# Kernel tuning notes

Measured on AMD Instinct MI355X. Metric: run time of the kernel, lower is better.

The kernel has to match this reference:

```python
import jax, jax.numpy as jnp
import numpy as np

EPS = 1e-6

def _conv(x, w, padding):
    # x: [B,C,H,W], w: [O,I,kh,kw]
    return jax.lax.conv_general_dilated(x, w, window_strides=(1, 1), padding=padding,
                                        dimension_numbers=('NCHW', 'OIHW', 'NCHW'))

def setup_inputs() -> dict:
    key = jax.random.key(0)
    ks = jax.random.split(key, 8)
    C = 512
    B, H, W = 4, 64, 64
    s1 = 1.0 / np.sqrt(C)          # 1x1 conv fan-in
    s3 = 1.0 / np.sqrt(C * 9)      # 3x3 conv fan-in
    return {
        'x': jax.random.normal(ks[0], (B, C, H, W), dtype=jnp.float32),
        'ln_w': jnp.ones((C,), dtype=jnp.float32),
        'ln_b': jnp.zeros((C,), dtype=jnp.float32),
        'wq': jax.random.normal(ks[1], (C, C, 1, 1), dtype=jnp.float32) * s1,
        'wk': jax.random.normal(ks[2], (C, C, 3, 3), dtype=jnp.float32) * s3,
        'wv': jax.random.normal(ks[3], (C, C, 3, 3), dtype=jnp.float32) * s3,
        'wp': jax.random.normal(ks[4], (C, C, 1, 1), dtype=jnp.float32) * s1,
        'bp': jnp.zeros((C,), dtype=jnp.float32),
    }

def reference(x, ln_w, ln_b, wq, wk, wv, wp, bp):
    # channels_first LayerNorm over C
    u = jnp.mean(x, axis=1, keepdims=True)
    s = jnp.mean((x - u) ** 2, axis=1, keepdims=True)
    h = (x - u) / jnp.sqrt(s + EPS)
    h = ln_w[None, :, None, None] * h + ln_b[None, :, None, None]

    q = _conv(h, wq, 'VALID')           # 1x1
    k = _conv(h, wk, [(1, 1), (1, 1)])  # 3x3, pad 1
    v = _conv(h, wv, [(1, 1), (1, 1)])

    b, c, H, W = q.shape
    hw = H * W
    q = q.reshape(b, c, hw)
    k = k.reshape(b, c, hw)
    v = v.reshape(b, c, hw)

    scale = jnp.asarray(int(c) ** (-0.5), q.dtype)
    attn = jnp.einsum('bcm,bcn->bmn', q, k) * scale  # [b, hw_q, hw_k]
    attn = jax.nn.softmax(attn, axis=2)
    out = jnp.einsum('bcn,bmn->bcm', v, attn)        # [b, c, hw_q]
    out = out.reshape(b, c, H, W)

    out = _conv(out, wp, 'VALID') + bp[None, :, None, None]
    return x + out
```

## Files before the change

### kernel.cpp

```cpp
#include <hip/hip_runtime.h>
#include <hip/hip_bf16.h>

#define C_DIM 512
#define HW    4096
#define BATCH 4
#define PW    66
#define PPIX  (PW*PW)

typedef __attribute__((ext_vector_type(8))) short bf16x8;
typedef __attribute__((ext_vector_type(4))) float f32x4;
typedef __attribute__((ext_vector_type(16))) float f32x16;
typedef __attribute__((ext_vector_type(2))) long long l64x2;

static __device__ __forceinline__ short f2b(float f) {
    union { float f; unsigned u; } v; v.f = f;
    unsigned r = v.u + 0x7fffu + ((v.u >> 16) & 1u);
    return (short)(r >> 16);
}
static __device__ __forceinline__ float b2f(short s) {
    union { unsigned u; float f; } v; v.u = ((unsigned)(unsigned short)s) << 16;
    return v.f;
}

static __device__ __forceinline__ f32x4 zero4() {
    f32x4 v = {0.f, 0.f, 0.f, 0.f};
    return v;
}
static __device__ __forceinline__ f32x16 zero16() {
    f32x16 v = {0.f,0.f,0.f,0.f, 0.f,0.f,0.f,0.f, 0.f,0.f,0.f,0.f, 0.f,0.f,0.f,0.f};
    return v;
}

static __device__ __forceinline__ void gload16(const void* g, void* l) {
    __builtin_amdgcn_global_load_lds(
        (__attribute__((address_space(1))) void*)g,
        (__attribute__((address_space(3))) void*)l, 16, 0, 0);
}

__global__ void k_reorder_w38(const float* __restrict__ w, unsigned char* __restrict__ out) {
    int i = blockIdx.x * 256 + threadIdx.x;
    int o = i / 576;
    int p8 = (i - o * 576) * 8;
    int kc2 = p8 >> 6;
    int tap = kc2 >> 3;
    int p = p8 & 63;
    int g = (p >> 4) & 3, half = (p >> 3) & 1;
    int c0 = (kc2 & 7) * 64 + half * 32 + g * 8;
    const float* src = w + ((size_t)o * 512 + c0) * 9 + tap;
    float f0 = src[0] * 64.f, f1 = src[9] * 64.f, f2 = src[18] * 64.f, f3 = src[27] * 64.f;
    float f4 = src[36] * 64.f, f5 = src[45] * 64.f, f6 = src[54] * 64.f, f7 = src[63] * 64.f;
    int lo = __builtin_amdgcn_cvt_pk_fp8_f32(f0, f1, 0, false);
    lo     = __builtin_amdgcn_cvt_pk_fp8_f32(f2, f3, lo, true);
    int hi = __builtin_amdgcn_cvt_pk_fp8_f32(f4, f5, 0, false);
    hi     = __builtin_amdgcn_cvt_pk_fp8_f32(f6, f7, hi, true);
    *(uint2*)&out[(size_t)o * 4608 + p8] = make_uint2((unsigned)lo, (unsigned)hi);
}

__global__ void k_reorder_w18(const float* __restrict__ w, unsigned char* __restrict__ out) {
    int i = blockIdx.x * 256 + threadIdx.x;
    int o = i >> 6;
    int p8 = (i & 63) * 8;
    int grp = p8 >> 6;
    int p = p8 & 63;
    int g = (p >> 4) & 3, half = (p >> 3) & 1;
    int c0 = grp * 64 + half * 32 + g * 8;
    const float* src = w + (size_t)o * 512 + c0;
    int lo = __builtin_amdgcn_cvt_pk_fp8_f32(src[0] * 64.f, src[1] * 64.f, 0, false);
    lo     = __builtin_amdgcn_cvt_pk_fp8_f32(src[2] * 64.f, src[3] * 64.f, lo, true);
    int hi = __builtin_amdgcn_cvt_pk_fp8_f32(src[4] * 64.f, src[5] * 64.f, 0, false);
    hi     = __builtin_amdgcn_cvt_pk_fp8_f32(src[6] * 64.f, src[7] * 64.f, hi, true);
    *(uint2*)&out[(size_t)o * 512 + p8] = make_uint2((unsigned)lo, (unsigned)hi);
}

__global__ void k_cvt_k8(const short* __restrict__ in, unsigned char* __restrict__ out) {
    int i = blockIdx.x * 256 + threadIdx.x;
    int m = i >> 6;
    int p = (i & 63) * 8;
    int kcp = p >> 6, g = (p >> 4) & 3, half = (p >> 3) & 1;
    int chb = (kcp * 2 + half) * 32 + g * 8;
    bf16x8 v = *(const bf16x8*)&in[(size_t)m * 512 + chb];
    int lo = __builtin_amdgcn_cvt_pk_fp8_f32(b2f(v[0]), b2f(v[1]), 0, false);
    lo     = __builtin_amdgcn_cvt_pk_fp8_f32(b2f(v[2]), b2f(v[3]), lo, true);
    int hi = __builtin_amdgcn_cvt_pk_fp8_f32(b2f(v[4]), b2f(v[5]), 0, false);
    hi     = __builtin_amdgcn_cvt_pk_fp8_f32(b2f(v[6]), b2f(v[7]), hi, true);
    *(uint2*)&out[(size_t)m * 512 + p] = make_uint2((unsigned)lo, (unsigned)hi);
}

__global__ void k_ln_fused(const float* __restrict__ x, const float* __restrict__ lnw,
                           const float* __restrict__ lnb, unsigned char* __restrict__ hp8) {
    __shared__ float red[8][64];
    __shared__ float mean_s[64], rstd_s[64];
    __shared__ short tile[64][65];
    int bid = blockIdx.x;
    int y = bid & 63, b = bid >> 6;
    int t = threadIdx.x;
    int px = t & 63, cg = t >> 6;
    const float* xb = x + (size_t)b * C_DIM * HW + (size_t)y * 64;

    float s = 0.f, sq = 0.f;
    for (int c = cg * 128; c < cg * 128 + 128; ++c) {
        float v = xb[(size_t)c * HW + px];
        s += v; sq += v * v;
    }
    red[cg][px] = s;
    red[4 + cg][px] = sq;
    __syncthreads();
    if (t < 64) {
        float S = red[0][t] + red[1][t] + red[2][t] + red[3][t];
        float Q = red[4][t] + red[5][t] + red[6][t] + red[7][t];
        float mu  = S * (1.0f / C_DIM);
        float var = Q * (1.0f / C_DIM) - mu * mu;
        mean_s[t] = mu;
        rstd_s[t] = 1.0f / sqrtf(var + 1e-6f);
    }
    __syncthreads();
    float mu = mean_s[px], rs = rstd_s[px];
    int chn = t & 7, pxe = t >> 3;
    int clocal = (chn & 1) * 32 + ((chn >> 1) & 3) * 8;
    for (int ct = 0; ct < 8; ++ct) {
        int c0 = ct * 64;
        #pragma unroll
        for (int cc = 0; cc < 64; cc += 4) {
            int c = c0 + cc + cg;
            float v = xb[(size_t)c * HW + px];
            tile[cc + cg][px] = f2b((v - mu) * rs * lnw[c] + lnb[c]);
        }
        __syncthreads();
        #pragma unroll
        for (int h = 0; h < 2; ++h) {
            int pix = pxe + h * 32;
            float f0 = b2f(tile[clocal + 0][pix]);
            float f1 = b2f(tile[clocal + 1][pix]);
            float f2 = b2f(tile[clocal + 2][pix]);
            float f3 = b2f(tile[clocal + 3][pix]);
            float f4 = b2f(tile[clocal + 4][pix]);
            float f5 = b2f(tile[clocal + 5][pix]);
            float f6 = b2f(tile[clocal + 6][pix]);
            float f7 = b2f(tile[clocal + 7][pix]);
            int lo = __builtin_amdgcn_cvt_pk_fp8_f32(f0, f1, 0, false);
            lo     = __builtin_amdgcn_cvt_pk_fp8_f32(f2, f3, lo, true);
            int hi = __builtin_amdgcn_cvt_pk_fp8_f32(f4, f5, 0, false);
            hi     = __builtin_amdgcn_cvt_pk_fp8_f32(f6, f7, hi, true);
            size_t row = (size_t)b * PPIX + (size_t)(y + 1) * PW + 1 + pix;
            *(uint2*)&hp8[row * 512 + c0 + chn * 8] = make_uint2((unsigned)lo, (unsigned)hi);
        }
        __syncthreads();
    }
}

__global__ __launch_bounds__(256, 2) void k_gemm_kv8(
        const unsigned char* __restrict__ A8, const unsigned char* __restrict__ Bk8,
        const unsigned char* __restrict__ Bv8, short* __restrict__ OutK,
        short* __restrict__ OutV)
{
    __shared__ unsigned char Alds[2][10240];
    __shared__ unsigned char Bklds[2][10240];
    __shared__ unsigned char Bvlds[2][10240];
    int bid = blockIdx.x;
    int mt = bid & 31, nt = (bid >> 5) & 3, b = bid >> 7;
    int m0 = mt * 128, n0 = nt * 128;
    int t = threadIdx.x;
    int lane = t & 63, w = t >> 6;
    int wm = w >> 1, wn = w & 1;
    int g = lane >> 4, li = lane & 15;
    const unsigned char* Ab = A8 + (size_t)b * PPIX * 512;

    int srowv[3], schv[3];
    #pragma unroll
    for (int r = 0; r < 3; ++r) {
        int slot = r * 256 + t;
        int row = slot / 5;
        int ch = slot - row * 5;
        srowv[r] = row;
        schv[r] = (ch < 4) ? ch * 16 : 0;
    }
    bool act2 = (w < 2);

    f32x4 accK[4][4], accV[4][4];
    #pragma unroll
    for (int i = 0; i < 4; ++i)
        #pragma unroll
        for (int j = 0; j < 4; ++j) { accK[i][j] = zero4(); accV[i][j] = zero4(); }

    auto STAGE = [&](int bf, int kc2) {
        int tap = kc2 >> 3;
        int gofs = (kc2 & 7) * 64;
        int ty3 = tap / 3, tx3 = tap % 3;
        #pragma unroll
        for (int r = 0; r < 3; ++r) {
            if (r < 2 || act2) {
                int row = srowv[r];
                int m = m0 + row;
                int yy = m >> 6, xx = m & 63;
                int pp = (yy + ty3) * PW + xx + tx3;
                int dst = (r * 256 + t) * 16;
                gload16(Ab + (size_t)pp * 512 + gofs + schv[r], &Alds[bf][dst]);
                size_t gb = (size_t)(n0 + row) * 4608 + kc2 * 64 + schv[r];
                gload16(Bk8 + gb, &Bklds[bf][dst]);
                gload16(Bv8 + gb, &Bvlds[bf][dst]);
            }
        }
    };

    auto COMPUTE = [&](int bf) {
        l64x2 av[4], bk[4], bv[4];
        #pragma unroll
        for (int i = 0; i < 4; ++i)
            av[i] = *(const l64x2*)&Alds[bf][(wm * 64 + i * 16 + li) * 80 + g * 16];
        #pragma unroll
        for (int j = 0; j < 4; ++j)
            bk[j] = *(const l64x2*)&Bklds[bf][(wn * 64 + j * 16 + li) * 80 + g * 16];
        #pragma unroll
        for (int j = 0; j < 4; ++j)
            bv[j] = *(const l64x2*)&Bvlds[bf][(wn * 64 + j * 16 + li) * 80 + g * 16];
        #pragma unroll
        for (int h = 0; h < 2; ++h) {
            #pragma unroll
            for (int i = 0; i < 4; ++i)
                #pragma unroll
                for (int j = 0; j < 4; ++j)
                    accK[i][j] = __builtin_amdgcn_mfma_f32_16x16x32_fp8_fp8(
                        av[i][h], bk[j][h], accK[i][j], 0, 0, 0);
            #pragma unroll
            for (int i = 0; i < 4; ++i)
                #pragma unroll
                for (int j = 0; j < 4; ++j)
                    accV[i][j] = __builtin_amdgcn_mfma_f32_16x16x32_fp8_fp8(
                        av[i][h], bv[j][h], accV[i][j], 0, 0, 0);
        }
    };

    STAGE(0, 0);
    __syncthreads();
    int bf = 0;
    for (int kc2 = 0; kc2 < 72; ++kc2) {
        if (kc2 + 1 < 72) STAGE(bf ^ 1, kc2 + 1);
        COMPUTE(bf);
        __syncthreads();
        bf ^= 1;
    }

    const float SCL = 0.015625f;
    #pragma unroll
    for (int fm = 0; fm < 4; ++fm) {
        #pragma unroll
        for (int fn = 0; fn < 4; ++fn) {
            int mrow = m0 + wm * 64 + fm * 16 + g * 4;
            int ncol = n0 + wn * 64 + fn * 16 + li;
            #pragma unroll
            for (int i = 0; i < 4; ++i) {
                size_t dst = ((size_t)b * HW + mrow + i) * C_DIM + ncol;
                OutK[dst] = f2b(accK[fm][fn][i] * SCL);
            }
            size_t dstv = ((size_t)b * C_DIM + ncol) * HW + mrow;
            short4 sv = make_short4(f2b(accV[fm][fn][0] * SCL), f2b(accV[fm][fn][1] * SCL),
                                    f2b(accV[fm][fn][2] * SCL), f2b(accV[fm][fn][3] * SCL));
            *(short4*)(OutV + dstv) = sv;
        }
    }
}

__global__ __launch_bounds__(256, 2) void k_gemm_q8(
        const unsigned char* __restrict__ A8, const unsigned char* __restrict__ Bq8,
        short* __restrict__ OutQ)
{
    __shared__ unsigned char Alds[2][10240];
    __shared__ unsigned char Blds[2][10240];
    int bid = blockIdx.x;
    int mt = bid & 31, nt = (bid >> 5) & 3, b = bid >> 7;
    int m0 = mt * 128, n0 = nt * 128;
    int t = threadIdx.x;
    int lane = t & 63, w = t >> 6;
    int wm = w >> 1, wn = w & 1;
    int g = lane >> 4, li = lane & 15;
    const unsigned char* Ab = A8 + (size_t)b * PPIX * 512;

    int srowv[3], schv[3];
    #pragma unroll
    for (int r = 0; r < 3; ++r) {
        int slot = r * 256 + t;
        int row = slot / 5;
        int ch = slot - row * 5;
        srowv[r] = row;
        schv[r] = (ch < 4) ? ch * 16 : 0;
    }
    bool act2 = (w < 2);

    f32x4 accQ[4][4];
    #pragma unroll
    for (int i = 0; i < 4; ++i)
        #pragma unroll
        for (int j = 0; j < 4; ++j) accQ[i][j] = zero4();

    auto STAGE = [&](int bf, int kc2) {
        int gofs = kc2 * 64;
        #pragma unroll
        for (int r = 0; r < 3; ++r) {
            if (r < 2 || act2) {
                int row = srowv[r];
                int m = m0 + row;
                int yy = m >> 6, xx = m & 63;
                int pp = (yy + 1) * PW + xx + 1;
                int dst = (r * 256 + t) * 16;
                gload16(Ab + (size_t)pp * 512 + gofs + schv[r], &Alds[bf][dst]);
                gload16(Bq8 + (size_t)(n0 + row) * 512 + gofs + schv[r], &Blds[bf][dst]);
            }
        }
    };

    auto COMPUTE = [&](int bf) {
        l64x2 av[4], bq[4];
        #pragma unroll
        for (int i = 0; i < 4; ++i)
            av[i] = *(const l64x2*)&Alds[bf][(wm * 64 + i * 16 + li) * 80 + g * 16];
        #pragma unroll
        for (int j = 0; j < 4; ++j)
            bq[j] = *(const l64x2*)&Blds[bf][(wn * 64 + j * 16 + li) * 80 + g * 16];
        #pragma unroll
        for (int h = 0; h < 2; ++h)
            #pragma unroll
            for (int i = 0; i < 4; ++i)
                #pragma unroll
                for (int j = 0; j < 4; ++j)
                    accQ[i][j] = __builtin_amdgcn_mfma_f32_16x16x32_fp8_fp8(
                        av[i][h], bq[j][h], accQ[i][j], 0, 0, 0);
    };

    STAGE(0, 0);
    __syncthreads();
    int bf = 0;
    for (int kc2 = 0; kc2 < 8; ++kc2) {
        if (kc2 + 1 < 8) STAGE(bf ^ 1, kc2 + 1);
        COMPUTE(bf);
        __syncthreads();
        bf ^= 1;
    }

    const float SCL = 0.015625f;
    #pragma unroll
    for (int fm = 0; fm < 4; ++fm) {
        #pragma unroll
        for (int fn = 0; fn < 4; ++fn) {
            int mrow = m0 + wm * 64 + fm * 16 + g * 4;
            int ncol = n0 + wn * 64 + fn * 16 + li;
            #pragma unroll
            for (int i = 0; i < 4; ++i) {
                size_t dst = ((size_t)b * HW + mrow + i) * C_DIM + ncol;
                OutQ[dst] = f2b(accQ[fm][fn][i] * SCL);
            }
        }
    }
}

__global__ __launch_bounds__(256, 2) void k_gemm_p8(
        const unsigned char* __restrict__ A8, const unsigned char* __restrict__ Bp8,
        float* __restrict__ Out, const float* __restrict__ bias,
        const float* __restrict__ resid)
{
    __shared__ unsigned char Alds[2][10240];
    __shared__ unsigned char Blds[2][10240];
    int bid = blockIdx.x;
    int mt = bid & 31, nt = (bid >> 5) & 3, b = bid >> 7;
    int m0 = mt * 128, n0 = nt * 128;
    int t = threadIdx.x;
    int lane = t & 63, w = t >> 6;
    int wm = w >> 1, wn = w & 1;
    int g = lane >> 4, li = lane & 15;
    const unsigned char* Ab = A8 + (size_t)b * HW * 512;

    int srowv[3], schv[3];
    #pragma unroll
    for (int r = 0; r < 3; ++r) {
        int slot = r * 256 + t;
        int row = slot / 5;
        int ch = slot - row * 5;
        srowv[r] = row;
        schv[r] = (ch < 4) ? ch * 16 : 0;
    }
    bool act2 = (w < 2);

    f32x4 acc[4][4];
    #pragma unroll
    for (int i = 0; i < 4; ++i)
        #pragma unroll
        for (int j = 0; j < 4; ++j) acc[i][j] = zero4();

    auto STAGE = [&](int bf, int kc2) {
        int gofs = kc2 * 64;
        #pragma unroll
        for (int r = 0; r < 3; ++r) {
            if (r < 2 || act2) {
                int row = srowv[r];
                int dst = (r * 256 + t) * 16;
                gload16(Ab + (size_t)(m0 + row) * 512 + gofs + schv[r], &Alds[bf][dst]);
                gload16(Bp8 + (size_t)(n0 + row) * 512 + gofs + schv[r], &Blds[bf][dst]);
            }
        }
    };

    auto COMPUTE = [&](int bf) {
        l64x2 av[4], bp[4];
        #pragma unroll
        for (int i = 0; i < 4; ++i)
            av[i] = *(const l64x2*)&Alds[bf][(wm * 64 + i * 16 + li) * 80 + g * 16];
        #pragma unroll
        for (int j = 0; j < 4; ++j)
            bp[j] = *(const l64x2*)&Blds[bf][(wn * 64 + j * 16 + li) * 80 + g * 16];
        #pragma unroll
        for (int h = 0; h < 2; ++h)
            #pragma unroll
            for (int i = 0; i < 4; ++i)
                #pragma unroll
                for (int j = 0; j < 4; ++j)
                    acc[i][j] = __builtin_amdgcn_mfma_f32_16x16x32_fp8_fp8(
                        av[i][h], bp[j][h], acc[i][j], 0, 0, 0);
    };

    STAGE(0, 0);
    __syncthreads();
    int bf = 0;
    for (int kc2 = 0; kc2 < 8; ++kc2) {
        if (kc2 + 1 < 8) STAGE(bf ^ 1, kc2 + 1);
        COMPUTE(bf);
        __syncthreads();
        bf ^= 1;
    }

    const float SCL = 0.015625f;
    #pragma unroll
    for (int fm = 0; fm < 4; ++fm) {
        #pragma unroll
        for (int fn = 0; fn < 4; ++fn) {
            int mrow = m0 + wm * 64 + fm * 16 + g * 4;
            int ncol = n0 + wn * 64 + fn * 16 + li;
            size_t dst = ((size_t)b * C_DIM + ncol) * HW + mrow;
            float bb = bias[ncol];
            float4 xr = *(const float4*)(resid + dst);
            float4 o;
            o.x = acc[fm][fn][0] * SCL + bb + xr.x;
            o.y = acc[fm][fn][1] * SCL + bb + xr.y;
            o.z = acc[fm][fn][2] * SCL + bb + xr.z;
            o.w = acc[fm][fn][3] * SCL + bb + xr.w;
            *(float4*)(Out + dst) = o;
        }
    }
}

#define KT 32
#define NTILES 64
__global__ __launch_bounds__(512, 2) void k_attn(
        const short* __restrict__ qT, const unsigned char* __restrict__ kT8,
        const short* __restrict__ vg, short* __restrict__ O0,
        short* __restrict__ O1, float* __restrict__ L0, float* __restrict__ L1)
{
    __shared__ __align__(16) short pool[73728];
    unsigned char* Kp8 = (unsigned char*)pool;
    short* Vp = pool + 16384;
    short* Pp = pool + 57344;

    int bid0 = blockIdx.x;
    int bid = (bid0 & 7) * 32 + (bid0 >> 3);
    int qt = bid & 31, ks = (bid >> 5) & 1, b = bid >> 6;
    int m0 = qt * 128;
    int t = threadIdx.x, lane = t & 63, w = t >> 6;
    int g = lane >> 4, li = lane & 15;
    int l31 = lane & 31, l5 = lane >> 5;

    const unsigned char* kb8 = kT8 + ((size_t)b * HW + (size_t)ks * 2048) * 512;
    const short* vb = vg + (size_t)b * C_DIM * HW + ks * 2048;

    long long qf8[16];
    {
        const short* qrow = qT + ((size_t)b * HW + m0 + w * 16 + li) * C_DIM;
        #pragma unroll
        for (int kc = 0; kc < 16; ++kc) {
            bf16x8 qv = *(const bf16x8*)&qrow[kc * 32 + g * 8];
            int lo = __builtin_amdgcn_cvt_pk_fp8_f32(b2f(qv[0]), b2f(qv[1]), 0, false);
            lo     = __builtin_amdgcn_cvt_pk_fp8_f32(b2f(qv[2]), b2f(qv[3]), lo, true);
            int hi = __builtin_amdgcn_cvt_pk_fp8_f32(b2f(qv[4]), b2f(qv[5]), 0, false);
            hi     = __builtin_amdgcn_cvt_pk_fp8_f32(b2f(qv[6]), b2f(qv[7]), hi, true);
            qf8[kc] = ((long long)(unsigned)hi << 32) | (unsigned)lo;
        }
    }
    f32x16 oacc[8];
    #pragma unroll
    for (int a = 0; a < 8; ++a) oacc[a] = zero16();
    float lsum = 0.f;

    const unsigned char* ksrc8 = kb8 + (size_t)(t & 31) * 512 + (t >> 5) * 16;
    int voff[5];
    #pragma unroll
    for (int r = 0; r < 5; ++r) {
        int D = r * 512 + t;
        int ch = D / 5;
        int c  = D - ch * 5;
        voff[r] = (c < 4) ? ch * 4096 + c * 8 : 0;
    }

    const float SC = 0.044194173824159216f * 1.4426950408889634f;

    auto STAGE = [&](int buf, int nt) {
        int n0 = nt * KT;
        const unsigned char* kS = ksrc8 + (size_t)n0 * 512;
        unsigned char* kD = Kp8 + buf * 16384 + t * 16;
        gload16(kS, kD);
        gload16(kS + 256, kD + 8192);
        short* vD = Vp + buf * 20480 + t * 8;
        #pragma unroll
        for (int r = 0; r < 5; ++r)
            gload16(vb + voff[r] + n0, vD + r * 4096);
    };

    STAGE(0, 0);
    asm volatile("s_waitcnt vmcnt(0)" ::: "memory");
    __builtin_amdgcn_s_barrier();
    __builtin_amdgcn_sched_barrier(0);

    int buf = 0;
    for (int nt = 0; nt < NTILES; ++nt) {
        if (nt + 1 < NTILES) STAGE(buf ^ 1, nt + 1);

        const unsigned char* kbase8 = Kp8 + buf * 16384 + g * 512 + li * 16;
        f32x4 s0[2], s1[2];
        s0[0] = zero4(); s0[1] = zero4(); s1[0] = zero4(); s1[1] = zero4();
        __builtin_amdgcn_s_setprio(1);
        #pragma unroll
        for (int kcp = 0; kcp < 8; ++kcp) {
            #pragma unroll
            for (int fn = 0; fn < 2; ++fn) {
                l64x2 kv = *(const l64x2*)&kbase8[kcp * 2048 + fn * 256];
                s0[fn] = __builtin_amdgcn_mfma_f32_16x16x32_fp8_fp8(kv[0], qf8[2 * kcp],     s0[fn], 0, 0, 0);
                s1[fn] = __builtin_amdgcn_mfma_f32_16x16x32_fp8_fp8(kv[1], qf8[2 * kcp + 1], s1[fn], 0, 0, 0);
            }
        }
        __builtin_amdgcn_s_setprio(0);
        #pragma unroll
        for (int fn = 0; fn < 2; ++fn) {
            float e0 = exp2f((s0[fn][0] + s1[fn][0]) * SC);
            float e1 = exp2f((s0[fn][1] + s1[fn][1]) * SC);
            float e2 = exp2f((s0[fn][2] + s1[fn][2]) * SC);
            float e3 = exp2f((s0[fn][3] + s1[fn][3]) * SC);
            lsum += (e0 + e1) + (e2 + e3);
            union { __hip_bfloat162 h; unsigned u; } p01, p23;
            p01.h = __float22bfloat162_rn(make_float2(e0, e1));
            p23.h = __float22bfloat162_rn(make_float2(e2, e3));
            *(uint2*)&Pp[(w * 16 + li) * 40 + fn * 16 + g * 4] = make_uint2(p01.u, p23.u);
        }

        asm volatile("s_waitcnt lgkmcnt(0)" ::: "memory");
        __builtin_amdgcn_s_barrier();
        __builtin_amdgcn_sched_barrier(0);

        const short* vbase = Vp + buf * 20480 + (size_t)w * 64 * 40;
        bf16x8 vf[2][2];
        #pragma unroll
        for (int cht = 0; cht < 2; ++cht)
            #pragma unroll
            for (int kx = 0; kx < 2; ++kx)
                vf[cht][kx] = *(const bf16x8*)&vbase[(cht * 32 + l31) * 40 + kx * 16 + l5 * 8];
        __builtin_amdgcn_s_setprio(1);
        #pragma unroll
        for (int q2 = 0; q2 < 4; ++q2) {
            #pragma unroll
            for (int kx = 0; kx < 2; ++kx) {
                bf16x8 pf = *(const bf16x8*)&Pp[(q2 * 32 + l31) * 40 + kx * 16 + l5 * 8];
                oacc[q2 * 2 + 0] = __builtin_amdgcn_mfma_f32_32x32x16_bf16(vf[0][kx], pf, oacc[q2 * 2 + 0], 0, 0, 0);
                oacc[q2 * 2 + 1] = __builtin_amdgcn_mfma_f32_32x32x16_bf16(vf[1][kx], pf, oacc[q2 * 2 + 1], 0, 0, 0);
            }
        }
        __builtin_amdgcn_s_setprio(0);

        asm volatile("s_waitcnt vmcnt(0)" ::: "memory");
        __builtin_amdgcn_s_barrier();
        __builtin_amdgcn_sched_barrier(0);
        buf ^= 1;
    }

    lsum += __shfl_xor(lsum, 16);
    lsum += __shfl_xor(lsum, 32);
    float* Lb = (ks ? L1 : L0) + (size_t)b * HW + m0 + w * 16;
    if (lane < 16) Lb[lane] = lsum;

    short* tp = pool + w * 9216;
    #pragma unroll
    for (int a = 0; a < 8; ++a) {
        int q2 = a >> 1, cht = a & 1;
        int q_l = q2 * 32 + l31;
        #pragma unroll
        for (int rq = 0; rq < 4; ++rq) {
            int chb = cht * 32 + rq * 8 + l5 * 4;
            union { __hip_bfloat162 h; unsigned u; } x01, x23;
            x01.h = __float22bfloat162_rn(make_float2(oacc[a][rq * 4 + 0], oacc[a][rq * 4 + 1]));
            x23.h = __float22bfloat162_rn(make_float2(oacc[a][rq * 4 + 2], oacc[a][rq * 4 + 3]));
            *(uint2*)&tp[q_l * 72 + chb] = make_uint2(x01.u, x23.u);
        }
    }
    asm volatile("s_waitcnt lgkmcnt(0)" ::: "memory");
    __builtin_amdgcn_sched_barrier(0);
    short* Ob = (ks ? O1 : O0) + ((size_t)b * HW + m0) * C_DIM + w * 64;
    #pragma unroll
    for (int qg = 0; qg < 16; ++qg) {
        int qr = qg * 8 + (lane >> 3);
        bf16x8 v = *(const bf16x8*)&tp[qr * 72 + (lane & 7) * 8];
        *(bf16x8*)&Ob[(size_t)qr * C_DIM + (lane & 7) * 8] = v;
    }
}

__global__ void k_att_comb(const short* __restrict__ O0, const short* __restrict__ O1,
                           const float* __restrict__ L0, const float* __restrict__ L1,
                           unsigned char* __restrict__ oatt8) {
    int i = blockIdx.x * 256 + threadIdx.x;
    int row = i >> 6;
    int cidx = i & 63;
    int c0 = cidx * 8;
    float r = 1.0f / (L0[row] + L1[row]);
    size_t base = (size_t)row * C_DIM + c0;
    bf16x8 a = *(const bf16x8*)&O0[base];
    bf16x8 c = *(const bf16x8*)&O1[base];
    float f[8];
    #pragma unroll
    for (int j = 0; j < 8; ++j)
        f[j] = (b2f(a[j]) + b2f(c[j])) * r;
    int lo = __builtin_amdgcn_cvt_pk_fp8_f32(f[0], f[1], 0, false);
    lo     = __builtin_amdgcn_cvt_pk_fp8_f32(f[2], f[3], lo, true);
    int hi = __builtin_amdgcn_cvt_pk_fp8_f32(f[4], f[5], 0, false);
    hi     = __builtin_amdgcn_cvt_pk_fp8_f32(f[6], f[7], hi, true);
    int pbyte = (cidx >> 3) * 64 + (cidx & 3) * 16 + ((cidx >> 2) & 1) * 8;
    *(uint2*)&oatt8[(size_t)row * 512 + pbyte] = make_uint2((unsigned)lo, (unsigned)hi);
}

extern "C" void kernel_launch(void* const* d_in, const int* in_sizes, int n_in,
                              void* d_out, int out_size, void* d_ws, size_t ws_size,
                              hipStream_t stream) {
    const float* x    = (const float*)d_in[0];
    const float* ln_w = (const float*)d_in[1];
    const float* ln_b = (const float*)d_in[2];
    const float* wq   = (const float*)d_in[3];
    const float* wk   = (const float*)d_in[4];
    const float* wv   = (const float*)d_in[5];
    const float* wp   = (const float*)d_in[6];
    const float* bp   = (const float*)d_in[7];
    float* out = (float*)d_out;

    char* ws = (char*)d_ws;
    size_t off = 0;
    auto alloc = [&](size_t bytes) {
        char* p = ws + off;
        off += (bytes + 255) & ~(size_t)255;
        return p;
    };
    short* hp   = (short*)alloc((size_t)BATCH * PPIX * C_DIM * 2);
    unsigned char* hp8 = (unsigned char*)alloc((size_t)BATCH * PPIX * 512);
    unsigned char* wq8 = (unsigned char*)alloc((size_t)512 * 512);
    unsigned char* wk8 = (unsigned char*)alloc((size_t)512 * 4608);
    unsigned char* wv8 = (unsigned char*)alloc((size_t)512 * 4608);
    unsigned char* wp8 = (unsigned char*)alloc((size_t)512 * 512);
    short* qT   = (short*)alloc((size_t)BATCH * HW * C_DIM * 2);
    short* kT   = (short*)alloc((size_t)BATCH * HW * C_DIM * 2);
    short* vg   = (short*)alloc((size_t)BATCH * HW * C_DIM * 2);
    short* oatt = (short*)alloc((size_t)BATCH * HW * C_DIM * 2);
    float* mean = (float*)alloc((size_t)BATCH * HW * 4);
    float* rstd = (float*)alloc((size_t)BATCH * HW * 4);

    hipMemsetAsync(hp8, 0, (size_t)BATCH * PPIX * 512, stream);
    k_reorder_w18<<<128, 256, 0, stream>>>(wq, wq8);
    k_reorder_w18<<<128, 256, 0, stream>>>(wp, wp8);
    k_reorder_w38<<<1152, 256, 0, stream>>>(wk, wk8);
    k_reorder_w38<<<1152, 256, 0, stream>>>(wv, wv8);
    k_ln_fused<<<256, 256, 0, stream>>>(x, ln_w, ln_b, hp8);

    k_gemm_q8<<<512, 256, 0, stream>>>(hp8, wq8, qT);
    k_gemm_kv8<<<512, 256, 0, stream>>>(hp8, wk8, wv8, kT, vg);

    unsigned char* kT8 = hp8;
    k_cvt_k8<<<4096, 256, 0, stream>>>(kT, kT8);

    short* Op0 = hp;
    short* Op1 = oatt;
    float* Ls0 = mean;
    float* Ls1 = rstd;
    k_attn<<<256, 512, 0, stream>>>(qT, kT8, vg, Op0, Op1, Ls0, Ls1);

    unsigned char* oatt8 = (unsigned char*)kT;
    k_att_comb<<<4096, 256, 0, stream>>>(Op0, Op1, Ls0, Ls1, oatt8);

    k_gemm_p8<<<512, 256, 0, stream>>>(oatt8, wp8, out, bp, x);
}
```

Before: 324.1 us.

## Store V in fp8 and retile attention to 64-query blocks of 256 threads

The KV GEMM now writes V as packed fp8 instead of bf16, halving V traffic and its shared-memory footprint in the attention kernel. The attention kernel is retiled from 512-thread blocks over 128 queries to 256-thread blocks over 64 queries, launched as twice as many blocks. Each wave now owns 128 channels and converts fp8 V back to bf16 in registers before the MFMA. This cuts LDS use per block and global load bytes, at the cost of extra conversion ALU work, lower V precision, and reloading K/V tiles for more query blocks.

```diff
diff --git a/kernel.cpp b/kernel.cpp
--- a/kernel.cpp
+++ b/kernel.cpp
@@ -11,6 +11,7 @@
 typedef __attribute__((ext_vector_type(4))) float f32x4;
 typedef __attribute__((ext_vector_type(16))) float f32x16;
 typedef __attribute__((ext_vector_type(2))) long long l64x2;
+typedef __attribute__((ext_vector_type(2))) float f32x2;
 
 static __device__ __forceinline__ short f2b(float f) {
     union { float f; unsigned u; } v; v.f = f;
@@ -151,7 +152,7 @@
 __global__ __launch_bounds__(256, 2) void k_gemm_kv8(
         const unsigned char* __restrict__ A8, const unsigned char* __restrict__ Bk8,
         const unsigned char* __restrict__ Bv8, short* __restrict__ OutK,
-        short* __restrict__ OutV)
+        unsigned char* __restrict__ OutV8)
 {
     __shared__ unsigned char Alds[2][10240];
     __shared__ unsigned char Bklds[2][10240];
@@ -253,9 +254,11 @@
                 OutK[dst] = f2b(accK[fm][fn][i] * SCL);
             }
             size_t dstv = ((size_t)b * C_DIM + ncol) * HW + mrow;
-            short4 sv = make_short4(f2b(accV[fm][fn][0] * SCL), f2b(accV[fm][fn][1] * SCL),
-                                    f2b(accV[fm][fn][2] * SCL), f2b(accV[fm][fn][3] * SCL));
-            *(short4*)(OutV + dstv) = sv;
+            int pk = __builtin_amdgcn_cvt_pk_fp8_f32(accV[fm][fn][0] * SCL,
+                                                     accV[fm][fn][1] * SCL, 0, false);
+            pk     = __builtin_amdgcn_cvt_pk_fp8_f32(accV[fm][fn][2] * SCL,
+                                                     accV[fm][fn][3] * SCL, pk, true);
+            *(unsigned*)&OutV8[dstv] = (unsigned)pk;
         }
     }
 }
@@ -448,26 +451,26 @@
 
 #define KT 32
 #define NTILES 64
-__global__ __launch_bounds__(512, 2) void k_attn(
+__global__ __launch_bounds__(256, 2) void k_attn(
         const short* __restrict__ qT, const unsigned char* __restrict__ kT8,
-        const short* __restrict__ vg, short* __restrict__ O0,
+        const unsigned char* __restrict__ vg8, short* __restrict__ O0,
         short* __restrict__ O1, float* __restrict__ L0, float* __restrict__ L1)
 {
-    __shared__ __align__(16) short pool[73728];
+    __shared__ __align__(16) short pool[35328];
     unsigned char* Kp8 = (unsigned char*)pool;
-    short* Vp = pool + 16384;
-    short* Pp = pool + 57344;
+    unsigned char* Vp8 = (unsigned char*)pool + 32768;
+    short* Pp = pool + 32768;
 
     int bid0 = blockIdx.x;
-    int bid = (bid0 & 7) * 32 + (bid0 >> 3);
-    int qt = bid & 31, ks = (bid >> 5) & 1, b = bid >> 6;
-    int m0 = qt * 128;
+    int bid = (bid0 & 7) * 64 + (bid0 >> 3);
+    int qt = bid & 63, ks = (bid >> 6) & 1, b = bid >> 7;
+    int m0 = qt * 64;
     int t = threadIdx.x, lane = t & 63, w = t >> 6;
     int g = lane >> 4, li = lane & 15;
     int l31 = lane & 31, l5 = lane >> 5;
 
     const unsigned char* kb8 = kT8 + ((size_t)b * HW + (size_t)ks * 2048) * 512;
-    const short* vb = vg + (size_t)b * C_DIM * HW + ks * 2048;
+    const unsigned char* vb8 = vg8 + (size_t)b * C_DIM * HW + ks * 2048;
 
     long long qf8[16];
     {
@@ -488,14 +491,7 @@
     float lsum = 0.f;
 
     const unsigned char* ksrc8 = kb8 + (size_t)(t & 31) * 512 + (t >> 5) * 16;
-    int voff[5];
-    #pragma unroll
-    for (int r = 0; r < 5; ++r) {
-        int D = r * 512 + t;
-        int ch = D / 5;
-        int c  = D - ch * 5;
-        voff[r] = (c < 4) ? ch * 4096 + c * 8 : 0;
-    }
+    const unsigned char* vsrc8 = vb8 + (size_t)(t >> 1) * 4096 + (t & 1) * 16;
 
     const float SC = 0.044194173824159216f * 1.4426950408889634f;
 
@@ -503,12 +499,13 @@
         int n0 = nt * KT;
         const unsigned char* kS = ksrc8 + (size_t)n0 * 512;
         unsigned char* kD = Kp8 + buf * 16384 + t * 16;
-        gload16(kS, kD);
-        gload16(kS + 256, kD + 8192);
-        short* vD = Vp + buf * 20480 + t * 8;
-        #pragma unroll
-        for (int r = 0; r < 5; ++r)
-            gload16(vb + voff[r] + n0, vD + r * 4096);
+        #pragma unroll
+        for (int r = 0; r < 4; ++r)
+            gload16(kS + r * 128, kD + r * 4096);
+        unsigned char* vD = Vp8 + buf * 16384 + t * 16;
+        #pragma unroll
+        for (int r = 0; r < 4; ++r)
+            gload16(vsrc8 + (size_t)r * 524288 + n0, vD + r * 4096);
     };
 
     STAGE(0, 0);
@@ -551,22 +548,41 @@
         __builtin_amdgcn_s_barrier();
         __builtin_amdgcn_sched_barrier(0);
 
-        const short* vbase = Vp + buf * 20480 + (size_t)w * 64 * 40;
-        bf16x8 vf[2][2];
-        #pragma unroll
-        for (int cht = 0; cht < 2; ++cht)
+        bf16x8 pf[2][2];
+        #pragma unroll
+        for (int q2 = 0; q2 < 2; ++q2)
             #pragma unroll
             for (int kx = 0; kx < 2; ++kx)
-                vf[cht][kx] = *(const bf16x8*)&vbase[(cht * 32 + l31) * 40 + kx * 16 + l5 * 8];
+                pf[q2][kx] = *(const bf16x8*)&Pp[(q2 * 32 + l31) * 40 + kx * 16 + l5 * 8];
+        const unsigned char* vbase8 = Vp8 + buf * 16384 + (w * 128 + l31) * 32 + l5 * 8;
         __builtin_amdgcn_s_setprio(1);
         #pragma unroll
-        for (int q2 = 0; q2 < 4; ++q2) {
+        for (int cht = 0; cht < 4; ++cht) {
+            bf16x8 vfb[2];
             #pragma unroll
             for (int kx = 0; kx < 2; ++kx) {
-                bf16x8 pf = *(const bf16x8*)&Pp[(q2 * 32 + l31) * 40 + kx * 16 + l5 * 8];
-                oacc[q2 * 2 + 0] = __builtin_amdgcn_mfma_f32_32x32x16_bf16(vf[0][kx], pf, oacc[q2 * 2 + 0], 0, 0, 0);
-                oacc[q2 * 2 + 1] = __builtin_amdgcn_mfma_f32_32x32x16_bf16(vf[1][kx], pf, oacc[q2 * 2 + 1], 0, 0, 0);
+                long long v8 = *(const long long*)&vbase8[cht * 1024 + kx * 16];
+                unsigned lo32 = (unsigned)(unsigned long long)v8;
+                unsigned hi32 = (unsigned)((unsigned long long)v8 >> 32);
+                f32x2 f01 = __builtin_amdgcn_cvt_pk_f32_fp8(lo32, false);
+                f32x2 f23 = __builtin_amdgcn_cvt_pk_f32_fp8(lo32, true);
+                f32x2 f45 = __builtin_amdgcn_cvt_pk_f32_fp8(hi32, false);
+                f32x2 f67 = __builtin_amdgcn_cvt_pk_f32_fp8(hi32, true);
+                union { __hip_bfloat162 h; unsigned u; } b01, b23, b45, b67;
+                b01.h = __float22bfloat162_rn(make_float2(f01[0], f01[1]));
+                b23.h = __float22bfloat162_rn(make_float2(f23[0], f23[1]));
+                b45.h = __float22bfloat162_rn(make_float2(f45[0], f45[1]));
+                b67.h = __float22bfloat162_rn(make_float2(f67[0], f67[1]));
+                union { bf16x8 v; unsigned u[4]; } vv;
+                vv.u[0] = b01.u; vv.u[1] = b23.u; vv.u[2] = b45.u; vv.u[3] = b67.u;
+                vfb[kx] = vv.v;
             }
+            #pragma unroll
+            for (int q2 = 0; q2 < 2; ++q2)
+                #pragma unroll
+                for (int kx = 0; kx < 2; ++kx)
+                    oacc[q2 * 4 + cht] = __builtin_amdgcn_mfma_f32_32x32x16_bf16(
+                        vfb[kx], pf[q2][kx], oacc[q2 * 4 + cht], 0, 0, 0);
         }
         __builtin_amdgcn_s_setprio(0);
 
@@ -581,10 +597,10 @@
     float* Lb = (ks ? L1 : L0) + (size_t)b * HW + m0 + w * 16;
     if (lane < 16) Lb[lane] = lsum;
 
-    short* tp = pool + w * 9216;
+    short* tp = pool + w * 8704;
     #pragma unroll
     for (int a = 0; a < 8; ++a) {
-        int q2 = a >> 1, cht = a & 1;
+        int q2 = a >> 2, cht = a & 3;
         int q_l = q2 * 32 + l31;
         #pragma unroll
         for (int rq = 0; rq < 4; ++rq) {
@@ -592,17 +608,17 @@
             union { __hip_bfloat162 h; unsigned u; } x01, x23;
             x01.h = __float22bfloat162_rn(make_float2(oacc[a][rq * 4 + 0], oacc[a][rq * 4 + 1]));
             x23.h = __float22bfloat162_rn(make_float2(oacc[a][rq * 4 + 2], oacc[a][rq * 4 + 3]));
-            *(uint2*)&tp[q_l * 72 + chb] = make_uint2(x01.u, x23.u);
+            *(uint2*)&tp[q_l * 136 + chb] = make_uint2(x01.u, x23.u);
         }
     }
     asm volatile("s_waitcnt lgkmcnt(0)" ::: "memory");
     __builtin_amdgcn_sched_barrier(0);
-    short* Ob = (ks ? O1 : O0) + ((size_t)b * HW + m0) * C_DIM + w * 64;
+    short* Ob = (ks ? O1 : O0) + ((size_t)b * HW + m0) * C_DIM + w * 128;
     #pragma unroll
     for (int qg = 0; qg < 16; ++qg) {
-        int qr = qg * 8 + (lane >> 3);
-        bf16x8 v = *(const bf16x8*)&tp[qr * 72 + (lane & 7) * 8];
-        *(bf16x8*)&Ob[(size_t)qr * C_DIM + (lane & 7) * 8] = v;
+        int qr = qg * 4 + (lane >> 4);
+        bf16x8 v = *(const bf16x8*)&tp[qr * 136 + (lane & 15) * 8];
+        *(bf16x8*)&Ob[(size_t)qr * C_DIM + (lane & 15) * 8] = v;
     }
 }
 
@@ -657,7 +673,7 @@
     unsigned char* wp8 = (unsigned char*)alloc((size_t)512 * 512);
     short* qT   = (short*)alloc((size_t)BATCH * HW * C_DIM * 2);
     short* kT   = (short*)alloc((size_t)BATCH * HW * C_DIM * 2);
-    short* vg   = (short*)alloc((size_t)BATCH * HW * C_DIM * 2);
+    unsigned char* vg8 = (unsigned char*)alloc((size_t)BATCH * C_DIM * HW);
     short* oatt = (short*)alloc((size_t)BATCH * HW * C_DIM * 2);
     float* mean = (float*)alloc((size_t)BATCH * HW * 4);
     float* rstd = (float*)alloc((size_t)BATCH * HW * 4);
@@ -670,7 +686,7 @@
     k_ln_fused<<<256, 256, 0, stream>>>(x, ln_w, ln_b, hp8);
 
     k_gemm_q8<<<512, 256, 0, stream>>>(hp8, wq8, qT);
-    k_gemm_kv8<<<512, 256, 0, stream>>>(hp8, wk8, wv8, kT, vg);
+    k_gemm_kv8<<<512, 256, 0, stream>>>(hp8, wk8, wv8, kT, vg8);
 
     unsigned char* kT8 = hp8;
     k_cvt_k8<<<4096, 256, 0, stream>>>(kT, kT8);
@@ -679,7 +695,7 @@
     short* Op1 = oatt;
     float* Ls0 = mean;
     float* Ls1 = rstd;
-    k_attn<<<256, 512, 0, stream>>>(qT, kT8, vg, Op0, Op1, Ls0, Ls1);
+    k_attn<<<512, 256, 0, stream>>>(qT, kT8, vg8, Op0, Op1, Ls0, Ls1);
 
     unsigned char* oatt8 = (unsigned char*)kT;
     k_att_comb<<<4096, 256, 0, stream>>>(Op0, Op1, Ls0, Ls1, oatt8);
```

After: 325.2 us. Within noise of the previous version (+0.3%).
